# Kernel tuning notes

Measured on AMD Instinct MI355X. Metric: run time of the kernel, lower is better.

The kernel has to match this reference:

```python
import jax, jax.numpy as jnp
import numpy as np

TEMP1 = 4.0  # self.temp1

def l2norm(x, eps=1e-8):
    # matches torch ref: x / (sqrt(sum(x^2)) + eps)
    return x / (jnp.sqrt(jnp.sum(x * x, axis=-1, keepdims=True)) + eps)

def setup_inputs() -> dict:
    key = jax.random.key(0)
    ks = jax.random.split(key, 8)
    B, C, H, W, D, Q = 32, 1024, 16, 16, 1000, 64
    return {
        "img_features_l": jax.random.normal(ks[0], (B, C, H, W), jnp.float32),
        "img_features_f": jax.random.normal(ks[1], (B, C, H, W), jnp.float32),
        "words_emb": jax.random.normal(ks[2], (B, D, Q), jnp.float32),
        "conv_w": jax.random.normal(ks[3], (D, C), jnp.float32) * 0.02,
        "conv_b": jnp.zeros((D,), jnp.float32),
        "sa_wl": jax.random.normal(ks[4], (D, D), jnp.float32) * 0.02,
        "sa_bl": jnp.zeros((D,), jnp.float32),
        "sa_wg": jax.random.normal(ks[5], (D, D), jnp.float32) * 0.02,
        "sa_bg": jnp.zeros((D,), jnp.float32),
        "sa_wc": jax.random.normal(ks[6], (D,), jnp.float32) * 0.05,
        "sa_bc": jnp.zeros((), jnp.float32),
        "cap_w": jax.random.normal(ks[7], (D,), jnp.float32) * 0.05,
        "cap_b": jnp.zeros((), jnp.float32),
    }

def reference(img_features_l, img_features_f, words_emb, conv_w, conv_b,
              sa_wl, sa_bl, sa_wg, sa_bg, sa_wc, sa_bc, cap_w, cap_b):
    B = img_features_f.shape[0]
    Bw = words_emb.shape[0]
    # 1x1 conv (1024 -> 1000), then flatten spatial and concat frontal+lateral
    f = jnp.einsum('oc,bchw->bohw', conv_w, img_features_f) + conv_b[None, :, None, None]
    l = jnp.einsum('oc,bchw->bohw', conv_w, img_features_l) + conv_b[None, :, None, None]
    img = jnp.concatenate([f.reshape(B, f.shape[1], -1),
                           l.reshape(B, l.shape[1], -1)], axis=2)  # [B, D, S]

    # attention_fn, vectorized over the per-word Python loop (axis i)
    # attn[i,b,s,q] = sum_d img[b,d,s] * words[i,d,q]
    logits = jnp.einsum('bds,idq->ibsq', img, words_emb)            # [Bw,B,S,Q]
    a1 = jax.nn.softmax(logits, axis=-1)                            # softmax over queryL
    a2 = jax.nn.softmax(jnp.swapaxes(a1, -1, -2) * TEMP1, axis=-1)  # [Bw,B,Q,S], softmax over sourceL
    # weightedContext (already transposed to [i,b,q,d])
    wctx = jnp.einsum('bds,ibqs->ibqd', img, a2)                    # [Bw,B,Q,D]

    word_t = jnp.swapaxes(words_emb, 1, 2)[:, None]                 # [Bw,1,Q,D]
    sim_loc = l2norm(wctx * word_t)                                 # [Bw,B,Q,D]
    sim_ave = jnp.mean(sim_loc, axis=2)                             # [Bw,B,D]

    # SA module (dropout in eval mode => identity)
    l_emb = jnp.tanh(jnp.einsum('ibqd,de->ibqe', sim_loc, sa_wl) + sa_bl)
    g_emb = jnp.tanh(jnp.einsum('ibd,de->ibe', sim_ave, sa_wg) + sa_bg)
    common = l_emb * g_emb[:, :, None, :]                           # [Bw,B,Q,D]
    w = jnp.einsum('ibqd,d->ibq', common, sa_wc) + sa_bc            # [Bw,B,Q]
    w = jax.nn.softmax(w, axis=-1)
    new_global = l2norm(jnp.einsum('ibq,ibqd->ibd', w, sim_loc))    # [Bw,B,D]
    sim = jax.nn.sigmoid(jnp.einsum('ibd,d->ib', new_global, cap_w) + cap_b)

    similarities_cap = sim.T                                        # [B, Bw]
    att_maps = a2[jnp.arange(Bw), jnp.arange(Bw)]                   # [Bw,Q,S] (attn[i] per word i)
    return similarities_cap, att_maps
```

## Files before the change

### kernel.cpp

```cpp
#include <hip/hip_runtime.h>
#include <cstdint>

typedef unsigned short u16;
typedef unsigned int   u32;
typedef __attribute__((ext_vector_type(8))) short bf16x8;
typedef __attribute__((ext_vector_type(4))) float f32x4;

#define D_DIM 1000
#define C_IN  1024
#define HW    256
#define S_DIM 512
#define Q_DIM 64

__device__ __forceinline__ u16 f2b(float x) {
    u32 u = __builtin_bit_cast(u32, x);
    u32 r = (u + 0x7FFFu + ((u >> 16) & 1u)) >> 16;
    return (u16)r;
}
__device__ __forceinline__ float b2f(u16 h) {
    u32 u = ((u32)h) << 16;
    return __builtin_bit_cast(float, u);
}
__device__ __forceinline__ float ftanh(float x) {
    float e = __expf(2.f * x);
    return 1.f - 2.f / (e + 1.f);
}

#define GLOAD(ldsptr, gptr) \
    __builtin_amdgcn_global_load_lds( \
        (const __attribute__((address_space(1))) unsigned int*)(gptr), \
        (__attribute__((address_space(3))) unsigned int*)(ldsptr), 16, 0, 0)

__global__ __launch_bounds__(256) void k_prepf(
    const float* __restrict__ feat_l, const float* __restrict__ feat_f,
    u16* __restrict__ fT_hi, u16* __restrict__ fT_lo)
{
    int bid = blockIdx.x;
    int ct = bid & 15, ht = (bid >> 4) & 3, half_ = (bid >> 6) & 1, b = bid >> 7;
    const float* src = (half_ ? feat_l : feat_f) + (size_t)b * C_IN * HW;
    __shared__ float T[64][65];
    int tid = threadIdx.x;
    {
        int cl = tid >> 2, h16 = (tid & 3) * 16;
        const float* p = src + (size_t)(ct * 64 + cl) * 256 + ht * 64 + h16;
        #pragma unroll
        for (int j = 0; j < 4; j++) {
            float4 v = *(const float4*)(p + j * 4);
            T[h16 + j * 4 + 0][cl] = v.x;
            T[h16 + j * 4 + 1][cl] = v.y;
            T[h16 + j * 4 + 2][cl] = v.z;
            T[h16 + j * 4 + 3][cl] = v.w;
        }
    }
    __syncthreads();
    {
        int hl = tid >> 2, c16 = (tid & 3) * 16;
        int srow = b * 512 + half_ * 256 + ht * 64 + hl;
        bf16x8 vh[2], vl[2];
        #pragma unroll
        for (int g = 0; g < 2; g++)
            #pragma unroll
            for (int j = 0; j < 8; j++) {
                float x = T[hl][c16 + g * 8 + j];
                u16 hh = f2b(x);
                vh[g][j] = (short)hh;
                vl[g][j] = (short)f2b(x - b2f(hh));
            }
        size_t o = (size_t)srow * 1024 + ct * 64 + c16;
        *(bf16x8*)(fT_hi + o) = vh[0];
        *(bf16x8*)(fT_hi + o + 8) = vh[1];
        *(bf16x8*)(fT_lo + o) = vl[0];
        *(bf16x8*)(fT_lo + o + 8) = vl[1];
    }
}

__global__ __launch_bounds__(256) void k_prepcw(
    const float* __restrict__ cw, u16* __restrict__ cwh, u16* __restrict__ cwl)
{
    int d = blockIdx.x;
    int c4 = threadIdx.x * 4;
    ushort4 h = make_ushort4(0, 0, 0, 0), lo = make_ushort4(0, 0, 0, 0);
    if (d < D_DIM) {
        float4 v = *(const float4*)(cw + (size_t)d * 1024 + c4);
        float a[4] = {v.x, v.y, v.z, v.w};
        u16* ph = (u16*)&h; u16* pl = (u16*)&lo;
        #pragma unroll
        for (int j = 0; j < 4; j++) {
            ph[j] = f2b(a[j]);
            pl[j] = f2b(a[j] - b2f(ph[j]));
        }
    }
    *(ushort4*)(cwh + (size_t)d * 1024 + c4) = h;
    *(ushort4*)(cwl + (size_t)d * 1024 + c4) = lo;
}

__global__ __launch_bounds__(256) void k_prepw(
    const float* __restrict__ words, u16* __restrict__ wth, u16* __restrict__ wtl)
{
    int i = blockIdx.x >> 4, dt = blockIdx.x & 15;
    const float* src = words + (size_t)i * D_DIM * Q_DIM;
    __shared__ u16 Th[64][72], Tl[64][72];
    int tid = threadIdx.x;
    #pragma unroll
    for (int rep = 0; rep < 4; rep++) {
        int idx = tid + rep * 256;
        int dl = idx >> 4, q4 = (idx & 15) * 4;
        int d = dt * 64 + dl;
        float4 v = make_float4(0.f, 0.f, 0.f, 0.f);
        if (d < D_DIM) v = *(const float4*)(src + (size_t)d * Q_DIM + q4);
        float a[4] = {v.x, v.y, v.z, v.w};
        #pragma unroll
        for (int jj = 0; jj < 4; jj++) {
            u16 hh = f2b(a[jj]);
            Th[dl][q4 + jj] = hh;
            Tl[dl][q4 + jj] = f2b(a[jj] - b2f(hh));
        }
    }
    __syncthreads();
    #pragma unroll
    for (int rep = 0; rep < 2; rep++) {
        int idx = tid + rep * 256;
        int q = idx >> 3, c8 = idx & 7;
        bf16x8 vh, vl;
        #pragma unroll
        for (int jj = 0; jj < 8; jj++) { vh[jj] = (short)Th[c8 * 8 + jj][q]; vl[jj] = (short)Tl[c8 * 8 + jj][q]; }
        size_t doff = (size_t)i * 65536 + (size_t)q * 1024 + dt * 64 + c8 * 8;
        *(bf16x8*)(wth + doff) = vh;
        *(bf16x8*)(wtl + doff) = vl;
    }
}

__global__ __launch_bounds__(256) void k_prep(const float* __restrict__ wl, u16* __restrict__ wlT)
{
    __shared__ float t[64][65];
    int bd = blockIdx.x & 15, be = blockIdx.x >> 4;
    int tx = threadIdx.x & 15, ty = threadIdx.x >> 4;
    #pragma unroll
    for (int rr = 0; rr < 4; rr++) {
        int r = ty * 4 + rr;
        int d = bd * 64 + r;
        int e4 = be * 64 + tx * 4;
        float v0 = 0.f, v1 = 0.f, v2 = 0.f, v3 = 0.f;
        if (d < D_DIM) {
            if (e4 + 3 < D_DIM) {
                float4 v = *reinterpret_cast<const float4*>(wl + (size_t)d * D_DIM + e4);
                v0 = v.x; v1 = v.y; v2 = v.z; v3 = v.w;
            } else {
                if (e4 + 0 < D_DIM) v0 = wl[(size_t)d * D_DIM + e4 + 0];
                if (e4 + 1 < D_DIM) v1 = wl[(size_t)d * D_DIM + e4 + 1];
                if (e4 + 2 < D_DIM) v2 = wl[(size_t)d * D_DIM + e4 + 2];
                if (e4 + 3 < D_DIM) v3 = wl[(size_t)d * D_DIM + e4 + 3];
            }
        }
        t[r][tx * 4 + 0] = v0; t[r][tx * 4 + 1] = v1;
        t[r][tx * 4 + 2] = v2; t[r][tx * 4 + 3] = v3;
    }
    __syncthreads();
    #pragma unroll
    for (int rr = 0; rr < 4; rr++) {
        int r2 = ty * 4 + rr;
        int e = be * 64 + r2;
        int d0 = bd * 64 + tx * 4;
        ushort4 h;
        h.x = f2b(t[tx * 4 + 0][r2]); h.y = f2b(t[tx * 4 + 1][r2]);
        h.z = f2b(t[tx * 4 + 2][r2]); h.w = f2b(t[tx * 4 + 3][r2]);
        *reinterpret_cast<ushort4*>(wlT + (size_t)e * 1024 + d0) = h;
    }
}

__global__ __launch_bounds__(512) void k_convG(
    const u16* __restrict__ fT_hi, const u16* __restrict__ fT_lo,
    const u16* __restrict__ cwh, const u16* __restrict__ cwl,
    const float* __restrict__ cb,
    u16* __restrict__ img_hi, u16* __restrict__ img_lo)
{
    const int bid = blockIdx.x;
    const int mblk = bid >> 2, nt = bid & 3;
    const int m0 = mblk * 256, n0 = nt * 256;

    __shared__ char LDS[131072] __attribute__((aligned(16)));
    __shared__ float cbS[256];

    const int tid = threadIdx.x;
    const int wid = tid >> 6, lane = tid & 63;
    const int wr = wid >> 2, wc = wid & 3;
    const int l15 = lane & 15, l4 = lane >> 4;
    const int sw = (l15 >> 1) & 3;

    if (tid < 256) {
        int d = n0 + tid;
        cbS[tid] = (d < D_DIM) ? cb[d] : 0.f;
    }

    auto stage = [&](int buf, int k0) {
        char* base = LDS + buf * 65536;
        #pragma unroll
        for (int rep = 0; rep < 2; rep++) {
            int idx = tid + rep * 512;
            int row = idx >> 2, slot = idx & 3;
            int kb = (slot ^ ((row >> 1) & 3)) * 16;
            size_t ao = (size_t)(m0 + row) * 2048 + (size_t)k0 * 2 + kb;
            size_t bo = (size_t)(n0 + row) * 2048 + (size_t)k0 * 2 + kb;
            GLOAD(base + idx * 16, (const char*)fT_hi + ao);
            GLOAD(base + 16384 + idx * 16, (const char*)fT_lo + ao);
            GLOAD(base + 32768 + idx * 16, (const char*)cwh + bo);
            GLOAD(base + 49152 + idx * 16, (const char*)cwl + bo);
        }
    };

    f32x4 acc[8][4] = {};

    stage(0, 0);
    __syncthreads();
    int cur = 0;
    for (int k0 = 0; k0 < 1024; k0 += 32) {
        if (k0 + 32 < 1024) stage(cur ^ 1, k0 + 32);
        const char* Ah = LDS + cur * 65536;
        const char* Alo = Ah + 16384;
        const char* Bh = Ah + 32768;
        const char* Blo = Ah + 49152;
        bf16x8 ah[8], bh[4];
        #pragma unroll
        for (int mf = 0; mf < 8; mf++)
            ah[mf] = *(const bf16x8*)(Ah + (wr * 128 + mf * 16 + l15) * 64 + ((l4 ^ sw) * 16));
        #pragma unroll
        for (int nf = 0; nf < 4; nf++)
            bh[nf] = *(const bf16x8*)(Bh + (wc * 64 + nf * 16 + l15) * 64 + ((l4 ^ sw) * 16));
        #pragma unroll
        for (int mf = 0; mf < 8; mf++)
            #pragma unroll
            for (int nf = 0; nf < 4; nf++)
                acc[mf][nf] = __builtin_amdgcn_mfma_f32_16x16x32_bf16(ah[mf], bh[nf], acc[mf][nf], 0, 0, 0);
        #pragma unroll
        for (int mf = 0; mf < 8; mf++) {
            bf16x8 al = *(const bf16x8*)(Alo + (wr * 128 + mf * 16 + l15) * 64 + ((l4 ^ sw) * 16));
            #pragma unroll
            for (int nf = 0; nf < 4; nf++)
                acc[mf][nf] = __builtin_amdgcn_mfma_f32_16x16x32_bf16(al, bh[nf], acc[mf][nf], 0, 0, 0);
        }
        #pragma unroll
        for (int nf = 0; nf < 4; nf++) {
            bf16x8 bl = *(const bf16x8*)(Blo + (wc * 64 + nf * 16 + l15) * 64 + ((l4 ^ sw) * 16));
            #pragma unroll
            for (int mf = 0; mf < 8; mf++)
                acc[mf][nf] = __builtin_amdgcn_mfma_f32_16x16x32_bf16(ah[mf], bl, acc[mf][nf], 0, 0, 0);
        }
        __syncthreads();
        cur ^= 1;
    }
    const int b = m0 >> 9;
    const int sbase = m0 & 511;
    #pragma unroll
    for (int mf = 0; mf < 8; mf++) {
        int srow = sbase + wr * 128 + mf * 16 + l4 * 4;
        #pragma unroll
        for (int nf = 0; nf < 4; nf++) {
            int dcol = n0 + wc * 64 + nf * 16 + l15;
            float bias = cbS[wc * 64 + nf * 16 + l15];
            ushort4 h4, lo4;
            u16* ph = (u16*)&h4; u16* pl = (u16*)&lo4;
            #pragma unroll
            for (int r = 0; r < 4; r++) {
                float v = acc[mf][nf][r] + bias;
                u16 hh = f2b(v);
                ph[r] = hh;
                pl[r] = f2b(v - b2f(hh));
            }
            size_t off = ((size_t)b * 1024 + dcol) * 512 + srow;
            *(ushort4*)(img_hi + off) = h4;
            *(ushort4*)(img_lo + off) = lo4;
        }
    }
}

__global__ __launch_bounds__(256) void k_trans(
    const u16* __restrict__ ih, const u16* __restrict__ il,
    u16* __restrict__ oth, u16* __restrict__ otl)
{
    int bid = blockIdx.x;
    int st = bid & 7, dt = (bid >> 3) & 15, b = bid >> 7;
    const u16* srcH = ih + (size_t)b * 1024 * 512;
    const u16* srcL = il + (size_t)b * 1024 * 512;
    u16* dstH = oth + (size_t)b * 512 * 1024;
    u16* dstL = otl + (size_t)b * 512 * 1024;
    __shared__ u16 Th[64][72], Tl[64][72];
    int tid = threadIdx.x;
    #pragma unroll
    for (int rep = 0; rep < 2; rep++) {
        int idx = tid + rep * 256;
        int dl = idx >> 3, c8 = idx & 7;
        size_t so = (size_t)(dt * 64 + dl) * 512 + st * 64 + c8 * 8;
        bf16x8 vh = *(const bf16x8*)(srcH + so);
        bf16x8 vl = *(const bf16x8*)(srcL + so);
        #pragma unroll
        for (int jj = 0; jj < 8; jj++) { Th[c8 * 8 + jj][dl] = (u16)vh[jj]; Tl[c8 * 8 + jj][dl] = (u16)vl[jj]; }
    }
    __syncthreads();
    #pragma unroll
    for (int rep = 0; rep < 2; rep++) {
        int idx = tid + rep * 256;
        int sl = idx >> 3, c8 = idx & 7;
        bf16x8 vh = *(const bf16x8*)(&Th[sl][c8 * 8]);
        bf16x8 vl = *(const bf16x8*)(&Tl[sl][c8 * 8]);
        size_t doff = (size_t)(st * 64 + sl) * 1024 + dt * 64 + c8 * 8;
        *(bf16x8*)(dstH + doff) = vh;
        *(bf16x8*)(dstL + doff) = vl;
    }
}

__global__ __launch_bounds__(512) void k_logits(
    const u16* __restrict__ wTh, const u16* __restrict__ wTl,
    const u16* __restrict__ iTh, const u16* __restrict__ iTl,
    u16* __restrict__ U, float* __restrict__ Zp, float* __restrict__ out)
{
    const int bid = blockIdx.x;
    const int b = bid >> 4, mt = (bid >> 1) & 7, nt = bid & 1;
    const int m0 = mt * 256, n0 = nt * 256;

    __shared__ char LDS[131072] __attribute__((aligned(16)));

    const int tid = threadIdx.x;
    const int wid = tid >> 6, lane = tid & 63;
    const int wr = wid >> 2, wc = wid & 3;
    const int l15 = lane & 15, l4 = lane >> 4;
    const int sw = (l15 >> 1) & 3;

    auto stage = [&](int buf, int k0) {
        char* base = LDS + buf * 65536;
        #pragma unroll
        for (int rep = 0; rep < 2; rep++) {
            int idx = tid + rep * 512;
            int row = idx >> 2, slot = idx & 3;
            int kb = (slot ^ ((row >> 1) & 3)) * 16;
            size_t ao = (size_t)(m0 + row) * 2048 + (size_t)k0 * 2 + kb;
            size_t bo = ((size_t)b * 512 + n0 + row) * 2048 + (size_t)k0 * 2 + kb;
            GLOAD(base + idx * 16, (const char*)wTh + ao);
            GLOAD(base + 16384 + idx * 16, (const char*)wTl + ao);
            GLOAD(base + 32768 + idx * 16, (const char*)iTh + bo);
            GLOAD(base + 49152 + idx * 16, (const char*)iTl + bo);
        }
    };

    f32x4 acc[8][4] = {};

    stage(0, 0);
    __syncthreads();
    int cur = 0;
    for (int k0 = 0; k0 < 1024; k0 += 32) {
        if (k0 + 32 < 1024) stage(cur ^ 1, k0 + 32);
        const char* Ah = LDS + cur * 65536;
        const char* Alo = Ah + 16384;
        const char* Bh = Ah + 32768;
        const char* Blo = Ah + 49152;
        bf16x8 ah[8], bh[4];
        #pragma unroll
        for (int mf = 0; mf < 8; mf++)
            ah[mf] = *(const bf16x8*)(Ah + (wr * 128 + mf * 16 + l15) * 64 + ((l4 ^ sw) * 16));
        #pragma unroll
        for (int nf = 0; nf < 4; nf++)
            bh[nf] = *(const bf16x8*)(Bh + (wc * 64 + nf * 16 + l15) * 64 + ((l4 ^ sw) * 16));
        #pragma unroll
        for (int mf = 0; mf < 8; mf++)
            #pragma unroll
            for (int nf = 0; nf < 4; nf++)
                acc[mf][nf] = __builtin_amdgcn_mfma_f32_16x16x32_bf16(ah[mf], bh[nf], acc[mf][nf], 0, 0, 0);
        #pragma unroll
        for (int mf = 0; mf < 8; mf++) {
            bf16x8 al = *(const bf16x8*)(Alo + (wr * 128 + mf * 16 + l15) * 64 + ((l4 ^ sw) * 16));
            #pragma unroll
            for (int nf = 0; nf < 4; nf++)
                acc[mf][nf] = __builtin_amdgcn_mfma_f32_16x16x32_bf16(al, bh[nf], acc[mf][nf], 0, 0, 0);
        }
        #pragma unroll
        for (int nf = 0; nf < 4; nf++) {
            bf16x8 bl = *(const bf16x8*)(Blo + (wc * 64 + nf * 16 + l15) * 64 + ((l4 ^ sw) * 16));
            #pragma unroll
            for (int mf = 0; mf < 8; mf++)
                acc[mf][nf] = __builtin_amdgcn_mfma_f32_16x16x32_bf16(ah[mf], bl, acc[mf][nf], 0, 0, 0);
        }
        __syncthreads();
        cur ^= 1;
    }

    float zacc[8][4] = {};
    #pragma unroll
    for (int il = 0; il < 2; il++) {
        int i_glob = mt * 4 + wr * 2 + il;
        bool diag = (i_glob == b);
        #pragma unroll
        for (int nf = 0; nf < 4; nf++) {
            int scol = n0 + wc * 64 + nf * 16 + l15;
            float m = -3.4e38f;
            #pragma unroll
            for (int mm = 0; mm < 4; mm++)
                #pragma unroll
                for (int r = 0; r < 4; r++)
                    m = fmaxf(m, acc[il * 4 + mm][nf][r]);
            m = fmaxf(m, __shfl_xor(m, 16));
            m = fmaxf(m, __shfl_xor(m, 32));
            float e[16], sum = 0.f;
            #pragma unroll
            for (int mm = 0; mm < 4; mm++)
                #pragma unroll
                for (int r = 0; r < 4; r++) {
                    float ev = __expf(acc[il * 4 + mm][nf][r] - m);
                    e[mm * 4 + r] = ev; sum += ev;
                }
            sum += __shfl_xor(sum, 16);
            sum += __shfl_xor(sum, 32);
            float inv = 1.f / sum;
            #pragma unroll
            for (int mm = 0; mm < 4; mm++)
                #pragma unroll
                for (int r = 0; r < 4; r++) {
                    float u = __expf(4.f * e[mm * 4 + r] * inv);
                    u16 ub = f2b(u);
                    zacc[il * 4 + mm][r] += b2f(ub);
                    int iqrow = m0 + wr * 128 + (il * 4 + mm) * 16 + l4 * 4 + r;
                    U[((size_t)b * 2048 + iqrow) * 512 + scol] = ub;
                    if (diag) {
                        int q = iqrow & 63;
                        out[1024 + ((size_t)i_glob * 64 + q) * 512 + scol] = u;
                    }
                }
        }
    }
    #pragma unroll
    for (int mf = 0; mf < 8; mf++)
        #pragma unroll
        for (int r = 0; r < 4; r++) {
            float z = zacc[mf][r];
            z += __shfl_xor(z, 1); z += __shfl_xor(z, 2);
            z += __shfl_xor(z, 4); z += __shfl_xor(z, 8);
            if (l15 == 0) {
                int iqrow = m0 + wr * 128 + mf * 16 + l4 * 4 + r;
                Zp[((size_t)b * 2048 + iqrow) * 8 + nt * 4 + wc] = z;
            }
        }
}

__global__ __launch_bounds__(256) void k_zred(const float* __restrict__ Zp, float* __restrict__ invZf)
{
    int gi = blockIdx.x * 256 + threadIdx.x;
    float4 z0 = *(const float4*)(Zp + (size_t)gi * 8);
    float4 z1 = *(const float4*)(Zp + (size_t)gi * 8 + 4);
    invZf[gi] = 1.f / (z0.x + z0.y + z0.z + z0.w + z1.x + z1.y + z1.z + z1.w);
}

__global__ __launch_bounds__(256) void k_attmap2(float* __restrict__ out)
{
    const int i = blockIdx.x;
    float* am = out + 1024 + (size_t)i * Q_DIM * S_DIM;
    int q = threadIdx.x >> 2, ch = threadIdx.x & 3;
    float s = 0.f;
    for (int ss = ch * 128; ss < ch * 128 + 128; ss++) s += am[(size_t)q * S_DIM + ss];
    s += __shfl_xor(s, 1);
    s += __shfl_xor(s, 2);
    float iz = 1.f / s;
    for (int ss = ch * 128; ss < ch * 128 + 128; ss++) am[(size_t)q * S_DIM + ss] *= iz;
}

__global__ __launch_bounds__(512) void k_wctx(
    const u16* __restrict__ img_hi, const u16* __restrict__ U,
    const float* __restrict__ invZf,
    const u16* __restrict__ wTh, const u16* __restrict__ wTl,
    u16* __restrict__ vbuf, float* __restrict__ ssqp)
{
    const int bid = blockIdx.x;
    const int b = bid >> 5, mt = (bid >> 3) & 3, nt = bid & 7;
    const int m0 = mt * 256, n0 = nt * 256;

    __shared__ char LDS[131072] __attribute__((aligned(16)));
    __shared__ float izS[256];

    const int tid = threadIdx.x;
    const int wid = tid >> 6, lane = tid & 63;
    const int wr = wid >> 2, wc = wid & 3;
    const int l15 = lane & 15, l4 = lane >> 4;
    const int sw = l15 & 7;

    if (tid < 256) izS[tid] = invZf[b * 2048 + n0 + tid];

    auto stage = [&](int buf, int k0) {
        char* base = LDS + buf * 65536;
        #pragma unroll
        for (int rep = 0; rep < 4; rep++) {
            int idx = tid + rep * 512;
            int row = idx >> 3, slot = idx & 7;
            int kb = (slot ^ (row & 7)) * 16;
            GLOAD(base + idx * 16, (const char*)img_hi + ((size_t)b * 1024 + m0 + row) * 1024 + (size_t)k0 * 2 + kb);
            GLOAD(base + 32768 + idx * 16, (const char*)U + ((size_t)b * 2048 + n0 + row) * 1024 + (size_t)k0 * 2 + kb);
        }
    };

    f32x4 acc[8][4] = {};

    stage(0, 0);
    __syncthreads();
    int cur = 0;
    for (int k0 = 0; k0 < 512; k0 += 64) {
        if (k0 + 64 < 512) stage(cur ^ 1, k0 + 64);
        const char* At = LDS + cur * 65536;
        const char* Bt = At + 32768;
        #pragma unroll
        for (int kf = 0; kf < 2; kf++) {
            bf16x8 a[8], bb[4];
            #pragma unroll
            for (int mf = 0; mf < 8; mf++)
                a[mf] = *(const bf16x8*)(At + (wr * 128 + mf * 16 + l15) * 128 + (((kf * 4 + l4) ^ sw) * 16));
            #pragma unroll
            for (int nf = 0; nf < 4; nf++)
                bb[nf] = *(const bf16x8*)(Bt + (wc * 64 + nf * 16 + l15) * 128 + (((kf * 4 + l4) ^ sw) * 16));
            #pragma unroll
            for (int mf = 0; mf < 8; mf++)
                #pragma unroll
                for (int nf = 0; nf < 4; nf++)
                    acc[mf][nf] = __builtin_amdgcn_mfma_f32_16x16x32_bf16(a[mf], bb[nf], acc[mf][nf], 0, 0, 0);
        }
        __syncthreads();
        cur ^= 1;
    }

    #pragma unroll
    for (int nf = 0; nf < 4; nf++) {
        int col = wc * 64 + nf * 16 + l15;
        int iq = n0 + col;
        float iz = izS[col];
        size_t wtoff = (size_t)iq * 1024;
        float s_nf = 0.f;
        #pragma unroll
        for (int mf = 0; mf < 8; mf++) {
            int d0 = m0 + wr * 128 + mf * 16 + l4 * 4;
            ushort4 wh = *(const ushort4*)(wTh + wtoff + d0);
            ushort4 wl = *(const ushort4*)(wTl + wtoff + d0);
            const u16* pwh = (const u16*)&wh;
            const u16* pwl = (const u16*)&wl;
            ushort4 vo;
            u16* pv = (u16*)&vo;
            #pragma unroll
            for (int r = 0; r < 4; r++) {
                float wv = b2f(pwh[r]) + b2f(pwl[r]);
                float v = acc[mf][nf][r] * iz * wv;
                s_nf = fmaf(v, v, s_nf);
                pv[r] = f2b(v);
            }
            *(ushort4*)(vbuf + ((size_t)b * 2048 + iq) * 1024 + d0) = vo;
        }
        s_nf += __shfl_xor(s_nf, 16);
        s_nf += __shfl_xor(s_nf, 32);
        if (l4 == 0) ssqp[((size_t)b * 2048 + iq) * 4 + mt] = s_nf;
    }
}

__global__ __launch_bounds__(256) void k_post(
    const u16* __restrict__ vbuf, const float* __restrict__ ssqp,
    float* __restrict__ invn_ws, u16* __restrict__ simave_bf)
{
    const int pair = blockIdx.x;
    __shared__ float invnS[64];
    const int tid = threadIdx.x;
    if (tid < 64) {
        size_t o = ((size_t)pair * 64 + tid) * 4;
        float s = ssqp[o] + ssqp[o + 1] + ssqp[o + 2] + ssqp[o + 3];
        float n = 1.f / (sqrtf(s) + 1e-8f);
        invnS[tid] = n;
        invn_ws[pair * 64 + tid] = n;
    }
    __syncthreads();
    int d0 = tid * 4;
    ushort4 o4 = make_ushort4(0, 0, 0, 0);
    if (d0 < D_DIM) {
        float a0 = 0.f, a1 = 0.f, a2 = 0.f, a3 = 0.f;
        const u16* vb = vbuf + (size_t)pair * 65536;
        for (int q = 0; q < 64; q++) {
            float n = invnS[q];
            ushort4 v = *(const ushort4*)(vb + q * 1024 + d0);
            a0 = fmaf(b2f(v.x), n, a0); a1 = fmaf(b2f(v.y), n, a1);
            a2 = fmaf(b2f(v.z), n, a2); a3 = fmaf(b2f(v.w), n, a3);
        }
        o4.x = f2b(a0 * (1.f / 64.f)); o4.y = f2b(a1 * (1.f / 64.f));
        o4.z = f2b(a2 * (1.f / 64.f)); o4.w = f2b(a3 * (1.f / 64.f));
    }
    *(ushort4*)(simave_bf + (size_t)pair * 1024 + d0) = o4;
}

__global__ __launch_bounds__(512) void k_g2M(
    const u16* __restrict__ simave_bf, const u16* __restrict__ wgT,
    const float* __restrict__ bg, const float* __restrict__ wc,
    float* __restrict__ g2)
{
    const int mt = blockIdx.x >> 2, nt = blockIdx.x & 3;
    const int m0 = mt * 256, n0 = nt * 256;

    __shared__ char LDS[131072] __attribute__((aligned(16)));
    __shared__ float bgS[256], wcS[256];

    const int tid = threadIdx.x;
    const int wid = tid >> 6, lane = tid & 63;
    const int wr = wid >> 2, wc_ = wid & 3;
    const int l15 = lane & 15, l4 = lane >> 4;
    const int sw = l15 & 7;

    if (tid < 256) {
        int e = n0 + tid;
        bgS[tid] = (e < D_DIM) ? bg[e] : 0.f;
        wcS[tid] = (e < D_DIM) ? wc[e] : 0.f;
    }

    auto stage = [&](int buf, int k0) {
        char* base = LDS + buf * 65536;
        #pragma unroll
        for (int rep = 0; rep < 4; rep++) {
            int idx = tid + rep * 512;
            int row = idx >> 3, slot = idx & 7;
            int kb = (slot ^ (row & 7)) * 16;
            GLOAD(base + idx * 16, (const char*)simave_bf + (size_t)(m0 + row) * 2048 + (size_t)k0 * 2 + kb);
            GLOAD(base + 32768 + idx * 16, (const char*)wgT + (size_t)(n0 + row) * 2048 + (size_t)k0 * 2 + kb);
        }
    };

    f32x4 acc[8][4] = {};

    stage(0, 0);
    __syncthreads();
    int cur = 0;
    for (int k0 = 0; k0 < 1024; k0 += 64) {
        if (k0 + 64 < 1024) stage(cur ^ 1, k0 + 64);
        const char* Al = LDS + cur * 65536;
        const char* Bl = Al + 32768;
        #pragma unroll
        for (int kf = 0; kf < 2; kf++) {
            bf16x8 a[8], bb[4];
            #pragma unroll
            for (int mf = 0; mf < 8; mf++)
                a[mf] = *(const bf16x8*)(Al + (wr * 128 + mf * 16 + l15) * 128 + (((kf * 4 + l4) ^ sw) * 16));
            #pragma unroll
            for (int nf = 0; nf < 4; nf++)
                bb[nf] = *(const bf16x8*)(Bl + (wc_ * 64 + nf * 16 + l15) * 128 + (((kf * 4 + l4) ^ sw) * 16));
            #pragma unroll
            for (int mf = 0; mf < 8; mf++)
                #pragma unroll
                for (int nf = 0; nf < 4; nf++)
                    acc[mf][nf] = __builtin_amdgcn_mfma_f32_16x16x32_bf16(a[mf], bb[nf], acc[mf][nf], 0, 0, 0);
        }
        __syncthreads();
        cur ^= 1;
    }

    #pragma unroll
    for (int mf = 0; mf < 8; mf++) {
        int p = m0 + wr * 128 + mf * 16 + l4 * 4;
        #pragma unroll
        for (int nf = 0; nf < 4; nf++) {
            int cl = wc_ * 64 + nf * 16 + l15;
            float bgv = bgS[cl], wcv = wcS[cl];
            #pragma unroll
            for (int r = 0; r < 4; r++)
                g2[(size_t)(p + r) * 1024 + n0 + cl] = ftanh(acc[mf][nf][r] + bgv) * wcv;
        }
    }
}

__global__ __launch_bounds__(512) void k_saG(
    const u16* __restrict__ vbuf, const u16* __restrict__ wlT,
    const float* __restrict__ invn_ws, const float* __restrict__ g2_ws,
    const float* __restrict__ bl, float* __restrict__ wspart)
{
    const int bid = blockIdx.x;
    const int wg = (bid & 7) * 128 + (bid >> 3);
    const int mt = wg >> 2, nt = wg & 3;
    const int m0 = mt * 256, n0 = nt * 256;

    __shared__ char LDS[131072] __attribute__((aligned(16)));
    __shared__ float invnS[256];
    __shared__ float blS[256];
    __shared__ float g2S[4 * 256];

    const int tid = threadIdx.x;
    const int wid = tid >> 6, lane = tid & 63;
    const int wr = wid >> 2, wc = wid & 3;
    const int l15 = lane & 15, l4 = lane >> 4;
    const int sw = l15 & 7;

    if (tid < 256) {
        invnS[tid] = invn_ws[m0 + tid];
        int e = n0 + tid;
        blS[tid] = (e < D_DIM) ? bl[e] : 0.f;
    }
    #pragma unroll
    for (int rep = 0; rep < 2; rep++) {
        int idx = tid + rep * 512;
        int p = idx >> 8, el = idx & 255;
        g2S[idx] = g2_ws[(size_t)((m0 >> 6) + p) * 1024 + n0 + el];
    }

    auto stage = [&](int buf, int k0) {
        char* base = LDS + buf * 65536;
        #pragma unroll
        for (int rep = 0; rep < 4; rep++) {
            int idx = tid + rep * 512;
            int row = idx >> 3, slot = idx & 7;
            int kb = (slot ^ (row & 7)) * 16;
            GLOAD(base + idx * 16, (const char*)vbuf + (size_t)(m0 + row) * 2048 + (size_t)k0 * 2 + kb);
            GLOAD(base + 32768 + idx * 16, (const char*)wlT + (size_t)(n0 + row) * 2048 + (size_t)k0 * 2 + kb);
        }
    };

    f32x4 acc[8][4] = {};

    stage(0, 0);
    __syncthreads();
    int cur = 0;
    for (int k0 = 0; k0 < 1024; k0 += 64) {
        if (k0 + 64 < 1024) stage(cur ^ 1, k0 + 64);
        const char* Al = LDS + cur * 65536;
        const char* Bl = Al + 32768;
        #pragma unroll
        for (int kf = 0; kf < 2; kf++) {
            bf16x8 a[8], bb[4];
            #pragma unroll
            for (int mf = 0; mf < 8; mf++)
                a[mf] = *(const bf16x8*)(Al + (wr * 128 + mf * 16 + l15) * 128 + (((kf * 4 + l4) ^ sw) * 16));
            #pragma unroll
            for (int nf = 0; nf < 4; nf++)
                bb[nf] = *(const bf16x8*)(Bl + (wc * 64 + nf * 16 + l15) * 128 + (((kf * 4 + l4) ^ sw) * 16));
            #pragma unroll
            for (int mf = 0; mf < 8; mf++)
                #pragma unroll
                for (int nf = 0; nf < 4; nf++)
                    acc[mf][nf] = __builtin_amdgcn_mfma_f32_16x16x32_bf16(a[mf], bb[nf], acc[mf][nf], 0, 0, 0);
        }
        __syncthreads();
        cur ^= 1;
    }

    #pragma unroll
    for (int mf = 0; mf < 8; mf++) {
        int mrow = wr * 128 + mf * 16 + l4 * 4;
        #pragma unroll
        for (int r = 0; r < 4; r++) {
            float inv = invnS[mrow + r];
            int p = (mrow + r) >> 6;
            float s = 0.f;
            #pragma unroll
            for (int nf = 0; nf < 4; nf++) {
                int el = wc * 64 + nf * 16 + l15;
                float x = acc[mf][nf][r] * inv + blS[el];
                s += ftanh(x) * g2S[p * 256 + el];
            }
            s += __shfl_xor(s, 1);
            s += __shfl_xor(s, 2);
            s += __shfl_xor(s, 4);
            s += __shfl_xor(s, 8);
            if (l15 == 0)
                wspart[(size_t)(nt * 4 + wc) * 65536 + m0 + mrow + r] = s;
        }
    }
}

__global__ __launch_bounds__(256) void k_sa2(
    const float* __restrict__ wspart, const float* __restrict__ invn_ws,
    const u16* __restrict__ vbuf, const float* __restrict__ capw,
    const float* __restrict__ capb, float* __restrict__ out)
{
    const int pair = blockIdx.x;
    const u16* vb = vbuf + (size_t)pair * 65536;

    __shared__ float wiS[64];
    __shared__ float red[8];

    const int tid = threadIdx.x;

    if (tid < 64) {
        float x = 0.f;
        #pragma unroll
        for (int c = 0; c < 16; c++) x += wspart[(size_t)c * 65536 + pair * 64 + tid];
        float m = x;
        #pragma unroll
        for (int mk = 1; mk < 64; mk <<= 1) m = fmaxf(m, __shfl_xor(m, mk));
        float e = __expf(x - m);
        float Z = e;
        #pragma unroll
        for (int mk = 1; mk < 64; mk <<= 1) Z += __shfl_xor(Z, mk);
        wiS[tid] = (e / Z) * invn_ws[pair * 64 + tid];
    }
    __syncthreads();

    float s1 = 0.f, s2 = 0.f;
    int d0 = tid * 4;
    if (d0 < D_DIM) {
        float a0 = 0.f, a1 = 0.f, a2 = 0.f, a3 = 0.f;
        for (int q = 0; q < 64; q++) {
            float wq = wiS[q];
            ushort4 v = *(const ushort4*)(vb + q * 1024 + d0);
            a0 = fmaf(wq, b2f(v.x), a0); a1 = fmaf(wq, b2f(v.y), a1);
            a2 = fmaf(wq, b2f(v.z), a2); a3 = fmaf(wq, b2f(v.w), a3);
        }
        float4 cw4 = *(const float4*)(capw + d0);
        s1 = a0 * cw4.x + a1 * cw4.y + a2 * cw4.z + a3 * cw4.w;
        s2 = a0 * a0 + a1 * a1 + a2 * a2 + a3 * a3;
    }
    #pragma unroll
    for (int mk = 1; mk < 64; mk <<= 1) { s1 += __shfl_xor(s1, mk); s2 += __shfl_xor(s2, mk); }
    if ((tid & 63) == 0) { red[tid >> 6] = s1; red[4 + (tid >> 6)] = s2; }
    __syncthreads();
    if (tid == 0) {
        float S1 = red[0] + red[1] + red[2] + red[3];
        float S2 = red[4] + red[5] + red[6] + red[7];
        float val = S1 / (sqrtf(S2) + 1e-8f) + capb[0];
        out[pair] = 1.f / (1.f + __expf(-val));
    }
}

extern "C" void kernel_launch(void* const* d_in, const int* in_sizes, int n_in,
                              void* d_out, int out_size, void* d_ws, size_t ws_size,
                              hipStream_t stream)
{
    const float* feat_l = (const float*)d_in[0];
    const float* feat_f = (const float*)d_in[1];
    const float* words  = (const float*)d_in[2];
    const float* conv_w = (const float*)d_in[3];
    const float* conv_b = (const float*)d_in[4];
    const float* sa_wl  = (const float*)d_in[5];
    const float* sa_bl  = (const float*)d_in[6];
    const float* sa_wg  = (const float*)d_in[7];
    const float* sa_bg  = (const float*)d_in[8];
    const float* sa_wc  = (const float*)d_in[9];
    const float* cap_w  = (const float*)d_in[11];
    const float* cap_b  = (const float*)d_in[12];
    float* out = (float*)d_out;

    char* ws = (char*)d_ws;
    u16*   featT_hi  = (u16*)(ws);
    u16*   featT_lo  = (u16*)(ws + 33554432);
    u16*   imgT_hi   = (u16*)(ws + 67108864);
    u16*   imgT_lo   = (u16*)(ws + 100663296);
    u16*   vbuf      = (u16*)(ws);
    u16*   img_hi    = (u16*)(ws + 134217728);
    u16*   wgT       = (u16*)(ws + 134217728);
    u16*   img_lo    = (u16*)(ws + 167772160);
    u16*   U         = (u16*)(ws + 167772160);
    float* wspart    = (float*)(ws + 167772160);
    u16*   wT_hi     = (u16*)(ws + 234881024);
    u16*   simave_bf = (u16*)(ws + 234881024);
    u16*   wT_lo     = (u16*)(ws + 239075328);
    u16*   cw_hi     = (u16*)(ws + 243269632);
    float* Zp        = (float*)(ws + 243269632);
    u16*   cw_lo     = (u16*)(ws + 245366784);
    float* invZf     = (float*)(ws + 245366784);
    float* ssqp      = (float*)(ws + 245628928);
    float* invn      = (float*)(ws + 246677504);
    u16*   wlT       = (u16*)(ws + 247463936);
    float* g2        = (float*)(ws + 249561088);

    hipLaunchKernelGGL(k_prepf, dim3(4096), dim3(256), 0, stream,
                       feat_l, feat_f, featT_hi, featT_lo);
    hipLaunchKernelGGL(k_prepcw, dim3(1024), dim3(256), 0, stream,
                       conv_w, cw_hi, cw_lo);
    hipLaunchKernelGGL(k_prepw, dim3(512), dim3(256), 0, stream,
                       words, wT_hi, wT_lo);
    hipLaunchKernelGGL(k_prep, dim3(256), dim3(256), 0, stream, sa_wl, wlT);
    hipLaunchKernelGGL(k_convG, dim3(256), dim3(512), 0, stream,
                       featT_hi, featT_lo, cw_hi, cw_lo, conv_b, img_hi, img_lo);
    hipLaunchKernelGGL(k_trans, dim3(4096), dim3(256), 0, stream,
                       img_hi, img_lo, imgT_hi, imgT_lo);
    hipLaunchKernelGGL(k_logits, dim3(512), dim3(512), 0, stream,
                       wT_hi, wT_lo, imgT_hi, imgT_lo, U, Zp, out);
    hipLaunchKernelGGL(k_zred, dim3(256), dim3(256), 0, stream, Zp, invZf);
    hipLaunchKernelGGL(k_attmap2, dim3(32), dim3(256), 0, stream, out);
    hipLaunchKernelGGL(k_wctx, dim3(1024), dim3(512), 0, stream,
                       img_hi, U, invZf, wT_hi, wT_lo, vbuf, ssqp);
    hipLaunchKernelGGL(k_prep, dim3(256), dim3(256), 0, stream, sa_wg, wgT);
    hipLaunchKernelGGL(k_post, dim3(1024), dim3(256), 0, stream,
                       vbuf, ssqp, invn, simave_bf);
    hipLaunchKernelGGL(k_g2M, dim3(16), dim3(512), 0, stream,
                       simave_bf, wgT, sa_bg, sa_wc, g2);
    hipLaunchKernelGGL(k_saG, dim3(1024), dim3(512), 0, stream,
                       vbuf, wlT, invn, g2, sa_bl, wspart);
    hipLaunchKernelGGL(k_sa2, dim3(1024), dim3(256), 0, stream,
                       wspart, invn, vbuf, cap_w, cap_b, out);
}
```

Measured before the change: 737.6 us.

## Fuse image transpose into conv GEMM epilogue, swizzle block order, retile g2 GEMM

The conv GEMM epilogue now writes only the bf16 high image plane in D-major layout. It also transposes the hi/lo split through LDS and writes it directly in S-major layout, which removes the separate k_trans kernel and its global round trip. Block indices in the conv, logits and wctx GEMMs are remapped in groups of eight, presumably to improve L2 locality across XCDs. The small g2 GEMM is retiled from 16 blocks of 256x256 to 64 blocks of 128x128 to fill more CUs. The cost is extra LDS passes and barriers in the conv epilogue.

```diff
diff --git a/kernel.cpp b/kernel.cpp
--- a/kernel.cpp
+++ b/kernel.cpp
@@ -172,9 +172,10 @@
     const u16* __restrict__ fT_hi, const u16* __restrict__ fT_lo,
     const u16* __restrict__ cwh, const u16* __restrict__ cwl,
     const float* __restrict__ cb,
-    u16* __restrict__ img_hi, u16* __restrict__ img_lo)
-{
-    const int bid = blockIdx.x;
+    u16* __restrict__ img_hi, u16* __restrict__ imgT_hi, u16* __restrict__ imgT_lo)
+{
+    const int bid0 = blockIdx.x;
+    const int bid = (bid0 & 7) * 32 + (bid0 >> 3);
     const int mblk = bid >> 2, nt = bid & 3;
     const int m0 = mblk * 256, n0 = nt * 256;
 
@@ -257,54 +258,46 @@
         for (int nf = 0; nf < 4; nf++) {
             int dcol = n0 + wc * 64 + nf * 16 + l15;
             float bias = cbS[wc * 64 + nf * 16 + l15];
-            ushort4 h4, lo4;
-            u16* ph = (u16*)&h4; u16* pl = (u16*)&lo4;
-            #pragma unroll
-            for (int r = 0; r < 4; r++) {
-                float v = acc[mf][nf][r] + bias;
-                u16 hh = f2b(v);
-                ph[r] = hh;
-                pl[r] = f2b(v - b2f(hh));
+            ushort4 h4;
+            u16* ph = (u16*)&h4;
+            #pragma unroll
+            for (int r = 0; r < 4; r++)
+                ph[r] = f2b(acc[mf][nf][r] + bias);
+            *(ushort4*)(img_hi + ((size_t)b * 1024 + dcol) * 512 + srow) = h4;
+        }
+    }
+    u16* Thi = (u16*)LDS;
+    u16* Tlo = (u16*)(LDS + 33792);
+    for (int qt = 0; qt < 4; qt++) {
+        __syncthreads();
+        if (wr == (qt >> 1)) {
+            #pragma unroll
+            for (int mm = 0; mm < 4; mm++) {
+                int mf = (qt & 1) * 4 + mm;
+                int sq = mm * 16 + l4 * 4;
+                #pragma unroll
+                for (int nf = 0; nf < 4; nf++) {
+                    int dcol = wc * 64 + nf * 16 + l15;
+                    float bias = cbS[dcol];
+                    #pragma unroll
+                    for (int r = 0; r < 4; r++) {
+                        float v = acc[mf][nf][r] + bias;
+                        u16 hh = f2b(v);
+                        Thi[(sq + r) * 264 + dcol] = hh;
+                        Tlo[(sq + r) * 264 + dcol] = f2b(v - b2f(hh));
+                    }
+                }
             }
-            size_t off = ((size_t)b * 1024 + dcol) * 512 + srow;
-            *(ushort4*)(img_hi + off) = h4;
-            *(ushort4*)(img_lo + off) = lo4;
-        }
-    }
-}
-
-__global__ __launch_bounds__(256) void k_trans(
-    const u16* __restrict__ ih, const u16* __restrict__ il,
-    u16* __restrict__ oth, u16* __restrict__ otl)
-{
-    int bid = blockIdx.x;
-    int st = bid & 7, dt = (bid >> 3) & 15, b = bid >> 7;
-    const u16* srcH = ih + (size_t)b * 1024 * 512;
-    const u16* srcL = il + (size_t)b * 1024 * 512;
-    u16* dstH = oth + (size_t)b * 512 * 1024;
-    u16* dstL = otl + (size_t)b * 512 * 1024;
-    __shared__ u16 Th[64][72], Tl[64][72];
-    int tid = threadIdx.x;
-    #pragma unroll
-    for (int rep = 0; rep < 2; rep++) {
-        int idx = tid + rep * 256;
-        int dl = idx >> 3, c8 = idx & 7;
-        size_t so = (size_t)(dt * 64 + dl) * 512 + st * 64 + c8 * 8;
-        bf16x8 vh = *(const bf16x8*)(srcH + so);
-        bf16x8 vl = *(const bf16x8*)(srcL + so);
-        #pragma unroll
-        for (int jj = 0; jj < 8; jj++) { Th[c8 * 8 + jj][dl] = (u16)vh[jj]; Tl[c8 * 8 + jj][dl] = (u16)vl[jj]; }
-    }
-    __syncthreads();
-    #pragma unroll
-    for (int rep = 0; rep < 2; rep++) {
-        int idx = tid + rep * 256;
-        int sl = idx >> 3, c8 = idx & 7;
-        bf16x8 vh = *(const bf16x8*)(&Th[sl][c8 * 8]);
-        bf16x8 vl = *(const bf16x8*)(&Tl[sl][c8 * 8]);
-        size_t doff = (size_t)(st * 64 + sl) * 1024 + dt * 64 + c8 * 8;
-        *(bf16x8*)(dstH + doff) = vh;
-        *(bf16x8*)(dstL + doff) = vl;
+        }
+        __syncthreads();
+        #pragma unroll
+        for (int rep = 0; rep < 4; rep++) {
+            int g = tid + rep * 512;
+            int s = g >> 5, d8 = (g & 31) * 8;
+            size_t go = ((size_t)b * 512 + sbase + qt * 64 + s) * 1024 + n0 + d8;
+            *(bf16x8*)(imgT_hi + go) = *(const bf16x8*)(&Thi[s * 264 + d8]);
+            *(bf16x8*)(imgT_lo + go) = *(const bf16x8*)(&Tlo[s * 264 + d8]);
+        }
     }
 }
 
@@ -313,7 +306,8 @@
     const u16* __restrict__ iTh, const u16* __restrict__ iTl,
     u16* __restrict__ U, float* __restrict__ Zp, float* __restrict__ out)
 {
-    const int bid = blockIdx.x;
+    const int bid0 = blockIdx.x;
+    const int bid = (bid0 & 7) * 64 + (bid0 >> 3);
     const int b = bid >> 4, mt = (bid >> 1) & 7, nt = bid & 1;
     const int m0 = mt * 256, n0 = nt * 256;
 
@@ -466,7 +460,8 @@
     const u16* __restrict__ wTh, const u16* __restrict__ wTl,
     u16* __restrict__ vbuf, float* __restrict__ ssqp)
 {
-    const int bid = blockIdx.x;
+    const int bid0 = blockIdx.x;
+    const int bid = (bid0 & 7) * 128 + (bid0 >> 3);
     const int b = bid >> 5, mt = (bid >> 3) & 3, nt = bid & 7;
     const int m0 = mt * 256, n0 = nt * 256;
 
@@ -584,61 +579,61 @@
     *(ushort4*)(simave_bf + (size_t)pair * 1024 + d0) = o4;
 }
 
-__global__ __launch_bounds__(512) void k_g2M(
+__global__ __launch_bounds__(256) void k_g2M(
     const u16* __restrict__ simave_bf, const u16* __restrict__ wgT,
     const float* __restrict__ bg, const float* __restrict__ wc,
     float* __restrict__ g2)
 {
-    const int mt = blockIdx.x >> 2, nt = blockIdx.x & 3;
-    const int m0 = mt * 256, n0 = nt * 256;
-
-    __shared__ char LDS[131072] __attribute__((aligned(16)));
-    __shared__ float bgS[256], wcS[256];
+    const int mt = blockIdx.x >> 3, nt = blockIdx.x & 7;
+    const int m0 = mt * 128, n0 = nt * 128;
+
+    __shared__ char LDS[65536] __attribute__((aligned(16)));
+    __shared__ float bgS[128], wcS[128];
 
     const int tid = threadIdx.x;
     const int wid = tid >> 6, lane = tid & 63;
-    const int wr = wid >> 2, wc_ = wid & 3;
+    const int wr = wid >> 1, wc_ = wid & 1;
     const int l15 = lane & 15, l4 = lane >> 4;
     const int sw = l15 & 7;
 
-    if (tid < 256) {
+    if (tid < 128) {
         int e = n0 + tid;
         bgS[tid] = (e < D_DIM) ? bg[e] : 0.f;
         wcS[tid] = (e < D_DIM) ? wc[e] : 0.f;
     }
 
     auto stage = [&](int buf, int k0) {
-        char* base = LDS + buf * 65536;
+        char* base = LDS + buf * 32768;
         #pragma unroll
         for (int rep = 0; rep < 4; rep++) {
-            int idx = tid + rep * 512;
+            int idx = tid + rep * 256;
             int row = idx >> 3, slot = idx & 7;
             int kb = (slot ^ (row & 7)) * 16;
             GLOAD(base + idx * 16, (const char*)simave_bf + (size_t)(m0 + row) * 2048 + (size_t)k0 * 2 + kb);
-            GLOAD(base + 32768 + idx * 16, (const char*)wgT + (size_t)(n0 + row) * 2048 + (size_t)k0 * 2 + kb);
+            GLOAD(base + 16384 + idx * 16, (const char*)wgT + (size_t)(n0 + row) * 2048 + (size_t)k0 * 2 + kb);
         }
     };
 
-    f32x4 acc[8][4] = {};
+    f32x4 acc[4][4] = {};
 
     stage(0, 0);
     __syncthreads();
     int cur = 0;
     for (int k0 = 0; k0 < 1024; k0 += 64) {
         if (k0 + 64 < 1024) stage(cur ^ 1, k0 + 64);
-        const char* Al = LDS + cur * 65536;
-        const char* Bl = Al + 32768;
+        const char* Al = LDS + cur * 32768;
+        const char* Bl = Al + 16384;
         #pragma unroll
         for (int kf = 0; kf < 2; kf++) {
-            bf16x8 a[8], bb[4];
-            #pragma unroll
-            for (int mf = 0; mf < 8; mf++)
-                a[mf] = *(const bf16x8*)(Al + (wr * 128 + mf * 16 + l15) * 128 + (((kf * 4 + l4) ^ sw) * 16));
+            bf16x8 a[4], bb[4];
+            #pragma unroll
+            for (int mf = 0; mf < 4; mf++)
+                a[mf] = *(const bf16x8*)(Al + (wr * 64 + mf * 16 + l15) * 128 + (((kf * 4 + l4) ^ sw) * 16));
             #pragma unroll
             for (int nf = 0; nf < 4; nf++)
                 bb[nf] = *(const bf16x8*)(Bl + (wc_ * 64 + nf * 16 + l15) * 128 + (((kf * 4 + l4) ^ sw) * 16));
             #pragma unroll
-            for (int mf = 0; mf < 8; mf++)
+            for (int mf = 0; mf < 4; mf++)
                 #pragma unroll
                 for (int nf = 0; nf < 4; nf++)
                     acc[mf][nf] = __builtin_amdgcn_mfma_f32_16x16x32_bf16(a[mf], bb[nf], acc[mf][nf], 0, 0, 0);
@@ -648,8 +643,8 @@
     }
 
     #pragma unroll
-    for (int mf = 0; mf < 8; mf++) {
-        int p = m0 + wr * 128 + mf * 16 + l4 * 4;
+    for (int mf = 0; mf < 4; mf++) {
+        int p = m0 + wr * 64 + mf * 16 + l4 * 4;
         #pragma unroll
         for (int nf = 0; nf < 4; nf++) {
             int cl = wc_ * 64 + nf * 16 + l15;
@@ -838,7 +833,6 @@
     u16*   vbuf      = (u16*)(ws);
     u16*   img_hi    = (u16*)(ws + 134217728);
     u16*   wgT       = (u16*)(ws + 134217728);
-    u16*   img_lo    = (u16*)(ws + 167772160);
     u16*   U         = (u16*)(ws + 167772160);
     float* wspart    = (float*)(ws + 167772160);
     u16*   wT_hi     = (u16*)(ws + 234881024);
@@ -861,9 +855,8 @@
                        words, wT_hi, wT_lo);
     hipLaunchKernelGGL(k_prep, dim3(256), dim3(256), 0, stream, sa_wl, wlT);
     hipLaunchKernelGGL(k_convG, dim3(256), dim3(512), 0, stream,
-                       featT_hi, featT_lo, cw_hi, cw_lo, conv_b, img_hi, img_lo);
-    hipLaunchKernelGGL(k_trans, dim3(4096), dim3(256), 0, stream,
-                       img_hi, img_lo, imgT_hi, imgT_lo);
+                       featT_hi, featT_lo, cw_hi, cw_lo, conv_b,
+                       img_hi, imgT_hi, imgT_lo);
     hipLaunchKernelGGL(k_logits, dim3(512), dim3(512), 0, stream,
                        wT_hi, wT_lo, imgT_hi, imgT_lo, U, Zp, out);
     hipLaunchKernelGGL(k_zred, dim3(256), dim3(256), 0, stream, Zp, invZf);
@@ -873,7 +866,7 @@
     hipLaunchKernelGGL(k_prep, dim3(256), dim3(256), 0, stream, sa_wg, wgT);
     hipLaunchKernelGGL(k_post, dim3(1024), dim3(256), 0, stream,
                        vbuf, ssqp, invn, simave_bf);
-    hipLaunchKernelGGL(k_g2M, dim3(16), dim3(512), 0, stream,
+    hipLaunchKernelGGL(k_g2M, dim3(64), dim3(256), 0, stream,
                        simave_bf, wgT, sa_bg, sa_wc, g2);
     hipLaunchKernelGGL(k_saG, dim3(1024), dim3(512), 0, stream,
                        vbuf, wlT, invn, g2, sa_bl, wspart);
```

After: 1.752 ms. 2.38x slower.
